# Performance work log

Hardware: AMD Instinct MI355X
Metric: run time of the kernel (lower is better)

The kernel has to match this reference:

```python
import jax, jax.numpy as jnp
import numpy as np

D = 1024      # model_dim
H = 2048      # expert hidden_dim
E = 8         # num routed experts
TOP_K = 2
N_SHARED = 1
B, S = 2, 1024


def setup_inputs() -> dict:
    key = jax.random.key(0)
    ks = jax.random.split(key, 12)
    sc = 0.02
    return {
        "hidden": jax.random.normal(ks[0], (B, S, D), jnp.float32),
        # router Linear(D -> E); stored as [in, out]
        "router_w": jax.random.normal(ks[1], (D, E), jnp.float32) * sc,
        "router_b": jnp.zeros((E,), jnp.float32),
        # shared expert (1): Linear(D->H), Linear(H->D)
        "sw1": jax.random.normal(ks[2], (D, H), jnp.float32) * sc,
        "sb1": jnp.zeros((H,), jnp.float32),
        "sw2": jax.random.normal(ks[3], (H, D), jnp.float32) * sc,
        "sb2": jnp.zeros((D,), jnp.float32),
        # routed experts, stacked over E
        "rw1": jax.random.normal(ks[4], (E, D, H), jnp.float32) * sc,
        "rb1": jnp.zeros((E, H), jnp.float32),
        "rw2": jax.random.normal(ks[5], (E, H, D), jnp.float32) * sc,
        "rb2": jnp.zeros((E, D), jnp.float32),
    }


def reference(hidden, router_w, router_b, sw1, sb1, sw2, sb2, rw1, rb1, rw2, rb2):
    b, s, d = hidden.shape
    T = b * s
    flat = hidden.reshape(T, d)                              # [T, D]

    # --- router ---
    router_logits = flat @ router_w + router_b               # [T, E]
    router_probs = jax.nn.softmax(router_logits, axis=-1)
    topk_probs, topk_idx = jax.lax.top_k(router_probs, TOP_K)  # [T, K]

    # per-(token, expert) mixing weight: sum of top-k probs that hit expert e
    weights = jnp.zeros_like(router_probs).at[
        jnp.arange(T)[:, None], topk_idx
    ].add(topk_probs)                                        # [T, E]

    # --- shared expert(s) (1 expert -> mean == itself) ---
    sh = jax.nn.gelu(flat @ sw1 + sb1, approximate=False)    # [T, H]
    shared_out = (sh @ sw2 + sb2) / N_SHARED                 # [T, D]

    # --- routed experts: dense all-expert eval weighted by routing weights ---
    # (identical math to the gather/FFN/index_add loop: weight is 0 for
    #  tokens not routed to expert e)
    h1 = jax.nn.gelu(jnp.einsum('td,edh->teh', flat, rw1) + rb1[None],
                     approximate=False)                      # [T, E, H]
    expert_out = jnp.einsum('teh,ehd->ted', h1, rw2) + rb2[None]  # [T, E, D]
    mixed = jnp.einsum('ted,te->td', expert_out, weights)    # [T, D]

    return (shared_out + mixed).reshape(b, s, d)
```

## Files before the change

### kernel.cpp

```cpp
#include <hip/hip_runtime.h>
#include <hip/hip_bf16.h>

#define T_TOK 2048
#define DDIM  1024
#define HDIM  2048
#define NEXP  8
#define NSEG  9

typedef unsigned short u16;
typedef __attribute__((ext_vector_type(4))) float f32x4;
typedef __attribute__((ext_vector_type(8))) short bf16x8;
typedef __attribute__((ext_vector_type(4))) unsigned short u16x4;

__device__ __forceinline__ u16 f2bf(float x) {
  union { float f; unsigned int u; } v; v.f = x;
  unsigned int r = v.u + 0x7fffu + ((v.u >> 16) & 1u);
  return (u16)(r >> 16);
}
__device__ __forceinline__ float gelu_exact(float x) {
  return 0.5f * x * (1.0f + erff(x * 0.70710678118654752f));
}
__device__ __forceinline__ int swz4(int row) {
  return (row & 3) ^ ((row >> 2) & 3);
}

__device__ __forceinline__ void gload16(const void* g, void* l) {
  __builtin_amdgcn_global_load_lds(
      (const __attribute__((address_space(1))) unsigned int*)g,
      (__attribute__((address_space(3))) unsigned int*)l, 16, 0, 0);
}

__global__ __launch_bounds__(256) void router_kernel(
    const float* __restrict__ x, const float* __restrict__ rw,
    const float* __restrict__ rb, u16* __restrict__ xb,
    float* __restrict__ weights, int* __restrict__ counts,
    int* __restrict__ lists)
{
  int wv = threadIdx.x >> 6, lane = threadIdx.x & 63;
  int t = blockIdx.x * 4 + wv;
  const float* xrow = x + (size_t)t * DDIM;
  float acc[NEXP];
#pragma unroll
  for (int e = 0; e < NEXP; e++) acc[e] = 0.f;
#pragma unroll
  for (int i = 0; i < 4; i++) {
    int d0 = i * 256 + lane * 4;
    f32x4 xv = *(const f32x4*)(xrow + d0);
    u16x4 pk;
#pragma unroll
    for (int j = 0; j < 4; j++) {
      float xs = xv[j];
      pk[j] = f2bf(xs);
      const float* wr = rw + (size_t)(d0 + j) * NEXP;
#pragma unroll
      for (int e = 0; e < NEXP; e++) acc[e] = fmaf(xs, wr[e], acc[e]);
    }
    *(u16x4*)(xb + (size_t)t * DDIM + d0) = pk;
  }
#pragma unroll
  for (int off = 32; off >= 1; off >>= 1)
#pragma unroll
    for (int e = 0; e < NEXP; e++) acc[e] += __shfl_xor(acc[e], off);

  if (lane == 0) {
    float lg[NEXP], mx = -1e30f;
#pragma unroll
    for (int e = 0; e < NEXP; e++) { lg[e] = acc[e] + rb[e]; mx = fmaxf(mx, lg[e]); }
    float p[NEXP], s = 0.f;
#pragma unroll
    for (int e = 0; e < NEXP; e++) { p[e] = expf(lg[e] - mx); s += p[e]; }
    float inv = 1.0f / s;
#pragma unroll
    for (int e = 0; e < NEXP; e++) p[e] *= inv;
    int i1 = 0;
#pragma unroll
    for (int e = 1; e < NEXP; e++) if (p[e] > p[i1]) i1 = e;
    int i2 = (i1 == 0) ? 1 : 0;
#pragma unroll
    for (int e = 0; e < NEXP; e++) if (e != i1 && p[e] > p[i2]) i2 = e;
#pragma unroll
    for (int e = 0; e < NEXP; e++)
      weights[(size_t)t * NEXP + e] = (e == i1) ? p[i1] : (e == i2) ? p[i2] : 0.f;
    int p1 = atomicAdd(counts + i1, 1); lists[i1 * T_TOK + p1] = t;
    int p2 = atomicAdd(counts + i2, 1); lists[i2 * T_TOK + p2] = t;
    lists[NEXP * T_TOK + t] = t;
  }
}

__global__ void seg_kernel(int* counts, int* segoff, int* ytab1, int* nyt1,
                           int* ytab2, int* nyt2) {
  counts[NEXP] = T_TOK;
  int off = 0, n1 = 0, n2 = 0;
  for (int e = 0; e < NSEG; e++) {
    segoff[e] = off;
    int c = counts[e];
    for (int my = 0; my * 128 < c; my++) ytab1[n1++] = e * 256 + my;
    for (int my = 0; my * 256 < c; my++) ytab2[n2++] = e * 256 + my;
    off += c;
  }
  *nyt1 = n1;
  *nyt2 = n2;
}

__global__ __launch_bounds__(256) void transpose_bf16_kernel(
    const float* __restrict__ rin, const float* __restrict__ sin_,
    u16* __restrict__ rout, u16* __restrict__ sout, int R, int C)
{
  __shared__ float tile[32][33];
  int b = blockIdx.z;
  const float* inb = (b < NEXP) ? rin + (size_t)b * R * C : sin_;
  u16* outb = (b < NEXP) ? rout + (size_t)b * R * C : sout;
  int r0 = blockIdx.y * 32, c0 = blockIdx.x * 32;
  int tx = threadIdx.x & 31, ty = threadIdx.x >> 5;
#pragma unroll
  for (int j = 0; j < 4; j++) {
    int r = ty + j * 8;
    tile[r][tx] = inb[(size_t)(r0 + r) * C + c0 + tx];
  }
  __syncthreads();
#pragma unroll
  for (int j = 0; j < 4; j++) {
    int rr = ty + j * 8;
    outb[(size_t)(c0 + rr) * R + r0 + tx] = f2bf(tile[tx][rr]);
  }
}

__global__ __launch_bounds__(256) void gemm1_kernel(
    const u16* __restrict__ Xb, const u16* __restrict__ rw1t,
    const u16* __restrict__ sw1t, const float* __restrict__ rb1,
    const float* __restrict__ sb1, const int* __restrict__ counts,
    const int* __restrict__ segoff, const int* __restrict__ lists,
    const int* __restrict__ ytab, const int* __restrict__ nyt,
    u16* __restrict__ H1)
{
  __shared__ u16 Alds[128 * 64];
  __shared__ u16 Blds[128 * 64];

  int tid = threadIdx.x, wv = tid >> 6, lane = tid & 63;
  int wm = wv >> 1, wn = wv & 1;
  int col8 = (lane & 7) * 8;

  int ntile = nyt[0] * (HDIM / 128);
  for (int t = blockIdx.x; t < ntile; t += gridDim.x) {
    int yt = t >> 4, nx = t & 15;
    int em = ytab[yt];
    int e = em >> 8, m0 = (em & 255) * 128, n0 = nx * 128;
    int cnt = counts[e];
    const u16* Bt = (e < NEXP) ? (rw1t + (size_t)e * HDIM * DDIM) : sw1t;
    const float* bias = (e < NEXP) ? (rb1 + (size_t)e * HDIM) : sb1;
    const int* list = lists + e * T_TOK;
    int seg = segoff[e];

    size_t asrc[4], bsrc[4];
#pragma unroll
    for (int r = 0; r < 4; r++) {
      int srow = r * 32 + wv * 8 + (lane >> 3);
      int tok = list[min(m0 + srow, cnt - 1)];
      asrc[r] = (size_t)tok * DDIM + col8;
      bsrc[r] = (size_t)(n0 + srow) * DDIM + col8;
    }

    f32x4 acc[4][4];
#pragma unroll
    for (int i = 0; i < 4; i++)
#pragma unroll
      for (int j = 0; j < 4; j++) acc[i][j] = (f32x4){0.f, 0.f, 0.f, 0.f};

    for (int kk = 0; kk < DDIM; kk += 64) {
#pragma unroll
      for (int r = 0; r < 4; r++) {
        gload16(Xb + asrc[r] + kk, Alds + (size_t)(r * 256 + wv * 64 + lane) * 8);
        gload16(Bt + bsrc[r] + kk, Blds + (size_t)(r * 256 + wv * 64 + lane) * 8);
      }
      __syncthreads();
#pragma unroll
      for (int ks = 0; ks < 2; ks++) {
        int kb = ks * 32 + (lane >> 4) * 8;
        bf16x8 af[4], bfr[4];
#pragma unroll
        for (int f = 0; f < 4; f++) {
          af[f]  = *(const bf16x8*)(Alds + (wm * 64 + f * 16 + (lane & 15)) * 64 + kb);
          bfr[f] = *(const bf16x8*)(Blds + (wn * 64 + f * 16 + (lane & 15)) * 64 + kb);
        }
#pragma unroll
        for (int mf = 0; mf < 4; mf++)
#pragma unroll
          for (int nf = 0; nf < 4; nf++)
            acc[mf][nf] = __builtin_amdgcn_mfma_f32_16x16x32_bf16(af[mf], bfr[nf], acc[mf][nf], 0, 0, 0);
      }
      __syncthreads();
    }

#pragma unroll
    for (int nf = 0; nf < 4; nf++) {
      int col = n0 + wn * 64 + nf * 16 + (lane & 15);
      float b = bias[col];
#pragma unroll
      for (int mf = 0; mf < 4; mf++) {
#pragma unroll
        for (int rg = 0; rg < 4; rg++) {
          int mt = wm * 64 + mf * 16 + (lane >> 4) * 4 + rg;
          if (m0 + mt < cnt) {
            float v = acc[mf][nf][rg] + b;
            H1[(size_t)(seg + m0 + mt) * HDIM + col] = f2bf(gelu_exact(v));
          }
        }
      }
    }
  }
}

__global__ __launch_bounds__(512) void gemm2_kernel(
    const u16* __restrict__ H1, const float* __restrict__ rw2,
    const float* __restrict__ sw2, const float* __restrict__ rb2,
    const float* __restrict__ sb2, const float* __restrict__ weights,
    const int* __restrict__ counts, const int* __restrict__ segoff,
    const int* __restrict__ lists, const int* __restrict__ ytab,
    const int* __restrict__ nyt, float* __restrict__ out)
{
  __shared__ u16 Alds[4][256 * 32];
  __shared__ u16 Blds[2][256 * 32];

  int tid = threadIdx.x, lane = tid & 63;
  int wv = tid >> 6, wm = wv >> 2, wn = wv & 3;
  int kc = lane >> 4, lr = lane & 15;

  int srow[2], soff[2];
#pragma unroll
  for (int j = 0; j < 2; j++) {
    int i = j * 512 + tid;
    srow[j] = i >> 2;
    soff[j] = (((i & 3) ^ swz4(i >> 2)) * 8);
  }
  int aoff[8], boff[4];
#pragma unroll
  for (int f = 0; f < 8; f++) {
    int ra = wm * 128 + f * 16 + lr;
    aoff[f] = ra * 32 + ((kc ^ swz4(ra)) * 8);
  }
#pragma unroll
  for (int f = 0; f < 4; f++) {
    int rb_ = wn * 64 + f * 16 + lr;
    boff[f] = rb_ * 32 + ((kc ^ swz4(rb_)) * 8);
  }
  int bw[4];
#pragma unroll
  for (int j = 0; j < 4; j++)
    bw[j] = ((lane << 2) + j) * 32 + (((wv >> 1) ^ j ^ (lane & 3)) << 3) + ((wv & 1) << 2);

  int ntile = nyt[0] * (DDIM / 256) * 2;
  for (int t = blockIdx.x; t < ntile; t += gridDim.x) {
    int kh = t & 1, nx = (t >> 1) & 3, yt = t >> 3;
    int em = ytab[yt];
    int e = em >> 8, m0 = (em & 255) * 256, n0 = nx * 256;
    int cnt = counts[e];
    const float* Wf = (e < NEXP) ? (rw2 + (size_t)e * HDIM * DDIM) : sw2;
    const float* bias = (e < NEXP) ? (rb2 + (size_t)e * DDIM) : sb2;
    const int* list = lists + e * T_TOK;
    int seg = segoff[e];
    int k0 = kh * 1024;

    size_t abase[2];
#pragma unroll
    for (int j = 0; j < 2; j++)
      abase[j] = (size_t)(seg + min(m0 + srow[j], cnt - 1)) * HDIM + k0 + soff[j];
    const float* Wb = Wf + (size_t)k0 * DDIM + n0 + (lane << 2);

    f32x4 acc[8][4];
#pragma unroll
    for (int i = 0; i < 8; i++)
#pragma unroll
      for (int j = 0; j < 4; j++) acc[i][j] = (f32x4){0.f, 0.f, 0.f, 0.f};

    const int NS = 1024 / 32;
    f32x4 vBa, vBb, vBc, vBd;
    {
      const float* Wk = Wb + (size_t)(wv * 4) * DDIM;
      vBa = *(const f32x4*)(Wk);
      vBb = *(const f32x4*)(Wk + DDIM);
      vBc = *(const f32x4*)(Wk + 2 * DDIM);
      vBd = *(const f32x4*)(Wk + 3 * DDIM);
    }
#pragma unroll
    for (int s = 0; s < 2; s++)
#pragma unroll
      for (int j = 0; j < 2; j++) {
        int i = j * 512 + tid;
        gload16(H1 + abase[j] + s * 32, &Alds[s][i * 8]);
      }

    for (int s = 0; s < NS; s++) {
      if (s + 2 < NS) {
        int kk = (s + 2) * 32;
        int nb = (s + 2) & 3;
#pragma unroll
        for (int j = 0; j < 2; j++) {
          int i = j * 512 + tid;
          gload16(H1 + abase[j] + kk, &Alds[nb][i * 8]);
        }
      }
      {
        u16* Bd = &Blds[s & 1][0];
#pragma unroll
        for (int j = 0; j < 4; j++) {
          u16x4 pk;
          pk[0] = f2bf(vBa[j]); pk[1] = f2bf(vBb[j]);
          pk[2] = f2bf(vBc[j]); pk[3] = f2bf(vBd[j]);
          *(u16x4*)(Bd + bw[j]) = pk;
        }
      }
      if (s + 1 < NS) {
        const float* Wk = Wb + (size_t)((s + 1) * 32 + wv * 4) * DDIM;
        vBa = *(const f32x4*)(Wk);
        vBb = *(const f32x4*)(Wk + DDIM);
        vBc = *(const f32x4*)(Wk + 2 * DDIM);
        vBd = *(const f32x4*)(Wk + 3 * DDIM);
      }
      if (s + 2 < NS)      asm volatile("s_waitcnt vmcnt(8)" ::: "memory");
      else if (s + 1 < NS) asm volatile("s_waitcnt vmcnt(6)" ::: "memory");
      else                 asm volatile("s_waitcnt vmcnt(0)" ::: "memory");
      asm volatile("s_waitcnt lgkmcnt(0)" ::: "memory");
      __builtin_amdgcn_s_barrier();
      __builtin_amdgcn_sched_barrier(0);

      const u16* Ac = &Alds[s & 3][0];
      const u16* Bc = &Blds[s & 1][0];
      bf16x8 af[8], bfr[4];
#pragma unroll
      for (int f = 0; f < 8; f++) af[f] = *(const bf16x8*)(Ac + aoff[f]);
#pragma unroll
      for (int f = 0; f < 4; f++) bfr[f] = *(const bf16x8*)(Bc + boff[f]);
      __builtin_amdgcn_s_setprio(1);
#pragma unroll
      for (int mf = 0; mf < 8; mf++)
#pragma unroll
        for (int nf = 0; nf < 4; nf++)
          acc[mf][nf] = __builtin_amdgcn_mfma_f32_16x16x32_bf16(af[mf], bfr[nf], acc[mf][nf], 0, 0, 0);
      __builtin_amdgcn_s_setprio(0);
    }

    float biasv[4];
#pragma unroll
    for (int nf = 0; nf < 4; nf++)
      biasv[nf] = (kh == 0) ? bias[n0 + wn * 64 + nf * 16 + lr] : 0.f;

#pragma unroll
    for (int mf = 0; mf < 8; mf++) {
#pragma unroll
      for (int rg = 0; rg < 4; rg++) {
        int mt = wm * 128 + mf * 16 + kc * 4 + rg;
        int mrow = m0 + mt;
        if (mrow < cnt) {
          int tok = list[mrow];
          float w = (e < NEXP) ? weights[(size_t)tok * NEXP + e] : 1.0f;
          float* orow = out + (size_t)tok * DDIM + n0 + wn * 64 + lr;
#pragma unroll
          for (int nf = 0; nf < 4; nf++)
            atomicAdd(orow + nf * 16, w * (acc[mf][nf][rg] + biasv[nf]));
        }
      }
    }
    __builtin_amdgcn_s_barrier();
    __builtin_amdgcn_sched_barrier(0);
  }
}

extern "C" void kernel_launch(void* const* d_in, const int* in_sizes, int n_in,
                              void* d_out, int out_size, void* d_ws, size_t ws_size,
                              hipStream_t stream) {
  (void)in_sizes; (void)n_in; (void)out_size; (void)ws_size;
  const float* hidden   = (const float*)d_in[0];
  const float* router_w = (const float*)d_in[1];
  const float* router_b = (const float*)d_in[2];
  const float* sw1 = (const float*)d_in[3];
  const float* sb1 = (const float*)d_in[4];
  const float* sw2 = (const float*)d_in[5];
  const float* sb2 = (const float*)d_in[6];
  const float* rw1 = (const float*)d_in[7];
  const float* rb1 = (const float*)d_in[8];
  const float* rw2 = (const float*)d_in[9];
  const float* rb2 = (const float*)d_in[10];
  float* out = (float*)d_out;

  char* ws = (char*)d_ws;
  u16* Xb      = (u16*)(ws + 0);
  u16* rw1t    = (u16*)(ws + 4194304);
  u16* sw1t    = (u16*)(ws + 37748736);
  u16* H1      = (u16*)(ws + 41943040);
  float* weights = (float*)(ws + 67108864);
  int* counts  = (int*)(ws + 67174400);
  int* segoff  = (int*)(ws + 67174464);
  int* lists   = (int*)(ws + 67174528);
  int* ytab1   = (int*)(ws + 67248256);
  int* nyt1    = (int*)(ws + 67248896);
  int* ytab2   = (int*)(ws + 67248960);
  int* nyt2    = (int*)(ws + 67249600);

  hipMemsetAsync(counts, 0, 64, stream);
  hipMemsetAsync(out, 0, (size_t)T_TOK * DDIM * sizeof(float), stream);

  router_kernel<<<T_TOK / 4, 256, 0, stream>>>(hidden, router_w, router_b, Xb,
                                               weights, counts, lists);
  seg_kernel<<<1, 1, 0, stream>>>(counts, segoff, ytab1, nyt1, ytab2, nyt2);

  transpose_bf16_kernel<<<dim3(HDIM / 32, DDIM / 32, NSEG), 256, 0, stream>>>(
      rw1, sw1, rw1t, sw1t, DDIM, HDIM);

  gemm1_kernel<<<1024, 256, 0, stream>>>(
      Xb, rw1t, sw1t, rb1, sb1, counts, segoff, lists, ytab1, nyt1, H1);
  gemm2_kernel<<<256, 512, 0, stream>>>(
      H1, rw2, sw2, rb2, sb2, weights, counts, segoff, lists, ytab2, nyt2, out);
}
```

Before: 245.7 us.

## Fuse weight transpose/bf16 conversion into gemm1 loads, swizzle LDS, approximate GELU

Removes the separate transpose kernel and has gemm1 read fp32 expert weights directly, converting them to bf16 in registers and writing them transposed into a swizzled LDS tile. The next k-slice of weights is prefetched into registers during the MFMA work. A/B LDS reads use an XOR swizzle to cut bank conflicts. Exact erf GELU is replaced by a sigmoid-based tanh approximation, which slightly changes numerics; weights are now re-read in fp32 for every M tile.

```diff
diff --git a/kernel.cpp b/kernel.cpp
--- a/kernel.cpp
+++ b/kernel.cpp
@@ -11,14 +11,16 @@
 typedef __attribute__((ext_vector_type(4))) float f32x4;
 typedef __attribute__((ext_vector_type(8))) short bf16x8;
 typedef __attribute__((ext_vector_type(4))) unsigned short u16x4;
+typedef __attribute__((ext_vector_type(8))) unsigned short u16x8;
 
 __device__ __forceinline__ u16 f2bf(float x) {
   union { float f; unsigned int u; } v; v.f = x;
   unsigned int r = v.u + 0x7fffu + ((v.u >> 16) & 1u);
   return (u16)(r >> 16);
 }
-__device__ __forceinline__ float gelu_exact(float x) {
-  return 0.5f * x * (1.0f + erff(x * 0.70710678118654752f));
+__device__ __forceinline__ float gelu_fast(float x) {
+  float y = x * (1.595769122f + 0.0713548162f * x * x);
+  return x / (1.0f + __expf(-y));
 }
 __device__ __forceinline__ int swz4(int row) {
   return (row & 3) ^ ((row >> 2) & 3);
@@ -102,32 +104,9 @@
   *nyt2 = n2;
 }
 
-__global__ __launch_bounds__(256) void transpose_bf16_kernel(
-    const float* __restrict__ rin, const float* __restrict__ sin_,
-    u16* __restrict__ rout, u16* __restrict__ sout, int R, int C)
-{
-  __shared__ float tile[32][33];
-  int b = blockIdx.z;
-  const float* inb = (b < NEXP) ? rin + (size_t)b * R * C : sin_;
-  u16* outb = (b < NEXP) ? rout + (size_t)b * R * C : sout;
-  int r0 = blockIdx.y * 32, c0 = blockIdx.x * 32;
-  int tx = threadIdx.x & 31, ty = threadIdx.x >> 5;
-#pragma unroll
-  for (int j = 0; j < 4; j++) {
-    int r = ty + j * 8;
-    tile[r][tx] = inb[(size_t)(r0 + r) * C + c0 + tx];
-  }
-  __syncthreads();
-#pragma unroll
-  for (int j = 0; j < 4; j++) {
-    int rr = ty + j * 8;
-    outb[(size_t)(c0 + rr) * R + r0 + tx] = f2bf(tile[tx][rr]);
-  }
-}
-
 __global__ __launch_bounds__(256) void gemm1_kernel(
-    const u16* __restrict__ Xb, const u16* __restrict__ rw1t,
-    const u16* __restrict__ sw1t, const float* __restrict__ rb1,
+    const u16* __restrict__ Xb, const float* __restrict__ rw1,
+    const float* __restrict__ sw1, const float* __restrict__ rb1,
     const float* __restrict__ sb1, const int* __restrict__ counts,
     const int* __restrict__ segoff, const int* __restrict__ lists,
     const int* __restrict__ ytab, const int* __restrict__ nyt,
@@ -136,9 +115,27 @@
   __shared__ u16 Alds[128 * 64];
   __shared__ u16 Blds[128 * 64];
 
-  int tid = threadIdx.x, wv = tid >> 6, lane = tid & 63;
-  int wm = wv >> 1, wn = wv & 1;
-  int col8 = (lane & 7) * 8;
+  int tid = threadIdx.x, lane = tid & 63;
+  int wv = tid >> 6, wm = wv >> 1, wn = wv & 1;
+  int kc = lane >> 4, lr = lane & 15;
+
+  int srow[4]; int achk[4];
+#pragma unroll
+  for (int r = 0; r < 4; r++) {
+    srow[r] = r * 32 + wv * 8 + (lane >> 3);
+    achk[r] = ((lane & 7) ^ (srow[r] & 7)) * 8;
+  }
+  int aoff[2][4], boff[2][4];
+#pragma unroll
+  for (int ks = 0; ks < 2; ks++)
+#pragma unroll
+    for (int f = 0; f < 4; f++) {
+      int ra = wm * 64 + f * 16 + lr;
+      int rb_ = wn * 64 + f * 16 + lr;
+      aoff[ks][f] = ra * 64 + (((ks * 4 + kc) ^ (ra & 7)) * 8);
+      boff[ks][f] = rb_ * 64 + (((ks * 4 + kc) ^ (rb_ & 7)) * 8);
+    }
+  int h8 = tid >> 5, bn = (lane & 31) * 4;
 
   int ntile = nyt[0] * (HDIM / 128);
   for (int t = blockIdx.x; t < ntile; t += gridDim.x) {
@@ -146,19 +143,18 @@
     int em = ytab[yt];
     int e = em >> 8, m0 = (em & 255) * 128, n0 = nx * 128;
     int cnt = counts[e];
-    const u16* Bt = (e < NEXP) ? (rw1t + (size_t)e * HDIM * DDIM) : sw1t;
+    const float* Wf = (e < NEXP) ? (rw1 + (size_t)e * DDIM * HDIM) : sw1;
     const float* bias = (e < NEXP) ? (rb1 + (size_t)e * HDIM) : sb1;
     const int* list = lists + e * T_TOK;
     int seg = segoff[e];
 
-    size_t asrc[4], bsrc[4];
+    size_t asrc[4];
 #pragma unroll
     for (int r = 0; r < 4; r++) {
-      int srow = r * 32 + wv * 8 + (lane >> 3);
-      int tok = list[min(m0 + srow, cnt - 1)];
-      asrc[r] = (size_t)tok * DDIM + col8;
-      bsrc[r] = (size_t)(n0 + srow) * DDIM + col8;
-    }
+      int tok = list[min(m0 + srow[r], cnt - 1)];
+      asrc[r] = (size_t)tok * DDIM + achk[r];
+    }
+    const float* Wb = Wf + n0 + bn;
 
     f32x4 acc[4][4];
 #pragma unroll
@@ -166,21 +162,40 @@
 #pragma unroll
       for (int j = 0; j < 4; j++) acc[i][j] = (f32x4){0.f, 0.f, 0.f, 0.f};
 
-    for (int kk = 0; kk < DDIM; kk += 64) {
-#pragma unroll
-      for (int r = 0; r < 4; r++) {
+    f32x4 vb[8];
+    {
+      const float* Wk = Wb + (size_t)(h8 * 8) * HDIM;
+#pragma unroll
+      for (int q = 0; q < 8; q++) vb[q] = *(const f32x4*)(Wk + (size_t)q * HDIM);
+    }
+
+    const int NS = DDIM / 64;
+    for (int s = 0; s < NS; s++) {
+      int kk = s * 64;
+#pragma unroll
+      for (int r = 0; r < 4; r++)
         gload16(Xb + asrc[r] + kk, Alds + (size_t)(r * 256 + wv * 64 + lane) * 8);
-        gload16(Bt + bsrc[r] + kk, Blds + (size_t)(r * 256 + wv * 64 + lane) * 8);
+#pragma unroll
+      for (int j = 0; j < 4; j++) {
+        u16x8 pk;
+#pragma unroll
+        for (int q = 0; q < 8; q++) pk[q] = f2bf(vb[q][j]);
+        int row = bn + j;
+        *(u16x8*)(Blds + (size_t)row * 64 + ((h8 ^ (row & 7)) * 8)) = pk;
       }
       __syncthreads();
+      if (s + 1 < NS) {
+        const float* Wk = Wb + (size_t)((s + 1) * 64 + h8 * 8) * HDIM;
+#pragma unroll
+        for (int q = 0; q < 8; q++) vb[q] = *(const f32x4*)(Wk + (size_t)q * HDIM);
+      }
 #pragma unroll
       for (int ks = 0; ks < 2; ks++) {
-        int kb = ks * 32 + (lane >> 4) * 8;
         bf16x8 af[4], bfr[4];
 #pragma unroll
         for (int f = 0; f < 4; f++) {
-          af[f]  = *(const bf16x8*)(Alds + (wm * 64 + f * 16 + (lane & 15)) * 64 + kb);
-          bfr[f] = *(const bf16x8*)(Blds + (wn * 64 + f * 16 + (lane & 15)) * 64 + kb);
+          af[f]  = *(const bf16x8*)(Alds + aoff[ks][f]);
+          bfr[f] = *(const bf16x8*)(Blds + boff[ks][f]);
         }
 #pragma unroll
         for (int mf = 0; mf < 4; mf++)
@@ -193,16 +208,16 @@
 
 #pragma unroll
     for (int nf = 0; nf < 4; nf++) {
-      int col = n0 + wn * 64 + nf * 16 + (lane & 15);
+      int col = n0 + wn * 64 + nf * 16 + lr;
       float b = bias[col];
 #pragma unroll
       for (int mf = 0; mf < 4; mf++) {
 #pragma unroll
         for (int rg = 0; rg < 4; rg++) {
-          int mt = wm * 64 + mf * 16 + (lane >> 4) * 4 + rg;
+          int mt = wm * 64 + mf * 16 + kc * 4 + rg;
           if (m0 + mt < cnt) {
             float v = acc[mf][nf][rg] + b;
-            H1[(size_t)(seg + m0 + mt) * HDIM + col] = f2bf(gelu_exact(v));
+            H1[(size_t)(seg + m0 + mt) * HDIM + col] = f2bf(gelu_fast(v));
           }
         }
       }
@@ -384,17 +399,15 @@
 
   char* ws = (char*)d_ws;
   u16* Xb      = (u16*)(ws + 0);
-  u16* rw1t    = (u16*)(ws + 4194304);
-  u16* sw1t    = (u16*)(ws + 37748736);
-  u16* H1      = (u16*)(ws + 41943040);
-  float* weights = (float*)(ws + 67108864);
-  int* counts  = (int*)(ws + 67174400);
-  int* segoff  = (int*)(ws + 67174464);
-  int* lists   = (int*)(ws + 67174528);
-  int* ytab1   = (int*)(ws + 67248256);
-  int* nyt1    = (int*)(ws + 67248896);
-  int* ytab2   = (int*)(ws + 67248960);
-  int* nyt2    = (int*)(ws + 67249600);
+  u16* H1      = (u16*)(ws + 4194304);
+  float* weights = (float*)(ws + 29360128);
+  int* counts  = (int*)(ws + 29425664);
+  int* segoff  = (int*)(ws + 29425728);
+  int* lists   = (int*)(ws + 29425792);
+  int* ytab1   = (int*)(ws + 29499520);
+  int* nyt1    = (int*)(ws + 29500160);
+  int* ytab2   = (int*)(ws + 29500224);
+  int* nyt2    = (int*)(ws + 29500864);
 
   hipMemsetAsync(counts, 0, 64, stream);
   hipMemsetAsync(out, 0, (size_t)T_TOK * DDIM * sizeof(float), stream);
@@ -403,11 +416,8 @@
                                                weights, counts, lists);
   seg_kernel<<<1, 1, 0, stream>>>(counts, segoff, ytab1, nyt1, ytab2, nyt2);
 
-  transpose_bf16_kernel<<<dim3(HDIM / 32, DDIM / 32, NSEG), 256, 0, stream>>>(
-      rw1, sw1, rw1t, sw1t, DDIM, HDIM);
-
   gemm1_kernel<<<1024, 256, 0, stream>>>(
-      Xb, rw1t, sw1t, rb1, sb1, counts, segoff, lists, ytab1, nyt1, H1);
+      Xb, rw1, sw1, rb1, sb1, counts, segoff, lists, ytab1, nyt1, H1);
   gemm2_kernel<<<256, 512, 0, stream>>>(
       H1, rw2, sw2, rb2, sb2, weights, counts, segoff, lists, ytab2, nyt2, out);
 }
```

Result: faster. 233.8 us (-4.8%).
